# Kernel tuning notes

Measured on AMD Instinct MI355X. Metric: run time of the kernel, lower is better.

The kernel has to match this reference:

```python
import jax, jax.numpy as jnp
import numpy as np

H, W, C, B = 96, 96, 21, 2
THETA_ALPHA, THETA_BETA, THETA_GAMMA = 160.0, 3.0, 3.0
N_ITERS = 5


def _coords():
    yy, xx = jnp.meshgrid(jnp.arange(H, dtype=jnp.float32),
                          jnp.arange(W, dtype=jnp.float32), indexing='ij')
    return jnp.stack([yy.ravel(), xx.ravel()], axis=-1)  # [N,2]


def _gauss_kernel(feat):
    # exact dense Gaussian kernel exp(-||fi-fj||^2/2); ground truth for the
    # permutohedral-lattice approximate high_dim_filter op.
    sq = jnp.sum(feat * feat, axis=-1)
    d2 = sq[:, None] + sq[None, :] - 2.0 * (feat @ feat.T)
    return jnp.exp(-0.5 * jnp.maximum(d2, 0.0))  # [N,N]


def setup_inputs():
    key = jax.random.key(0)
    k1, k2 = jax.random.split(key)
    unary = jax.random.normal(k1, (B, H, W, C), dtype=jnp.float32)
    rgb = jax.random.uniform(k2, (B, H, W, 3), dtype=jnp.float32) * 255.0
    return {
        'unary': unary,
        'rgb': rgb,
        'spatial_ker_weights': jnp.eye(C, dtype=jnp.float32),
        'bilateral_ker_weights': jnp.eye(C, dtype=jnp.float32),
        'compatibility_matrix': -jnp.eye(C, dtype=jnp.float32),
    }


def _crf_single(u_chw, rgb_chw, Ws, Wb, M):
    N = H * W
    pos = _coords()
    # filter op has no gradient w.r.t. guide features in the original custom op
    rgb_flat = jax.lax.stop_gradient(rgb_chw).reshape(3, N).T  # [N,3]
    Ks = _gauss_kernel(pos / THETA_GAMMA)                       # spatial kernel [N,N]
    Kb = _gauss_kernel(jnp.concatenate([pos / THETA_ALPHA,
                                        rgb_flat / THETA_BETA], axis=-1))  # bilateral [N,N]
    ones = jnp.ones((N,), dtype=jnp.float32)
    sn = Ks @ ones  # spatial norm vals (filter of all-ones)
    bn = Kb @ ones  # bilateral norm vals
    u = u_chw.reshape(C, N)
    q = u
    for _ in range(N_ITERS):
        sm = jax.nn.softmax(q, axis=0)   # softmax over classes, [C,N]
        sp = (sm @ Ks) / sn              # Ks symmetric -> filtering = sm @ Ks
        bl = (sm @ Kb) / bn
        msg = Ws @ sp + Wb @ bl          # learned message passing [C,N]
        q = u - M @ msg                  # compatibility transform + unary update
    return q  # [C,N]


def reference(unary, rgb, spatial_ker_weights, bilateral_ker_weights, compatibility_matrix):
    u = jnp.transpose(unary, (0, 3, 1, 2))  # [B,C,H,W]
    r = jnp.transpose(rgb, (0, 3, 1, 2))    # [B,3,H,W]
    q = jax.vmap(_crf_single, in_axes=(0, 0, None, None, None))(
        u, r, spatial_ker_weights, bilateral_ker_weights, compatibility_matrix)
    return jnp.transpose(q.reshape(B, C, H, W), (0, 2, 3, 1))  # [B,H,W,C]
```

## Files before the change

kernel.cpp:

```cpp
#include <hip/hip_runtime.h>

#define HH 96
#define WW 96
#define CC 21
#define BB 2
#define NN (HH*WW)
#define NT16 (NN/16)
#define NJB  (NN/32)
#define CHK 8
#define NBILB 1296
#define PRUNE_T 24.0f
#define GST 104

#define KSA2 (0.84932184f / 160.0f)
#define KSB2 (0.84932184f / 3.0f)
#define GL2  (1.44269504f / 18.0f)

typedef __attribute__((ext_vector_type(4))) float f32x4;
typedef __attribute__((ext_vector_type(8))) short short8;
typedef __attribute__((ext_vector_type(4))) int int4v;

static __device__ inline unsigned pk_bf16(float a, float b) {
    unsigned ua = __builtin_bit_cast(unsigned, a);
    unsigned ub = __builtin_bit_cast(unsigned, b);
    ua += 0x7FFF + ((ua >> 16) & 1);
    ub += 0x7FFF + ((ub >> 16) & 1);
    return (ua >> 16) | (ub & 0xFFFF0000u);
}
static __device__ inline unsigned short bf16_1(float a) {
    unsigned ua = __builtin_bit_cast(unsigned, a);
    ua += 0x7FFF + ((ua >> 16) & 1);
    return (unsigned short)(ua >> 16);
}

__global__ __launch_bounds__(256) void prep_kernel(
    float* __restrict__ sxt, unsigned short* __restrict__ gbt,
    unsigned short* __restrict__ smht, int* __restrict__ gh, int* __restrict__ wlc)
{
    int idx = blockIdx.x * 256 + threadIdx.x;
    if (idx == 0) wlc[0] = 0;
    if (idx < BB * 11 * NN) {
        int b = idx / (11 * NN);
        int rem = idx - b * 11 * NN;
        int r = rem / NN, col = rem - r * NN;
        smht[(size_t)(b * 32 + 21 + r) * NN + col] = (r == 0) ? 0x3F80 : 0;
    }
    if (idx < BB * 4096) gh[idx] = 0;
    if (blockIdx.x == 0) {
        __shared__ float gt[96];
        int t = threadIdx.x;
        if (t < 96) gt[t] = __builtin_amdgcn_exp2f(-(float)(t * t) * GL2);
        __syncthreads();
        if (t < 96) {
            float s = 0.f;
            for (int v = 0; v < 96; v++) s += gt[abs(t - v)];
            sxt[t] = s;
            for (int v = 0; v < 96; v++) gbt[t * 96 + v] = bf16_1(gt[abs(t - v)]);
        }
    }
}

__global__ __launch_bounds__(256) void hist_kernel(
    const float* __restrict__ rgb, int* __restrict__ gh)
{
    int idx = blockIdx.x * 256 + threadIdx.x;
    if (idx >= BB * NN) return;
    int b = idx / NN;
    const float* rp = rgb + (size_t)idx * 3;
    int cr = min(15, (int)rp[0] >> 4);
    int cg = min(15, (int)rp[1] >> 4);
    int cb = min(15, (int)rp[2] >> 4);
    atomicAdd(&gh[b * 4096 + ((cr << 8) | (cg << 4) | cb)], 1);
}

__global__ __launch_bounds__(256) void scan_kernel(
    const int* __restrict__ gh, int* __restrict__ goff)
{
    __shared__ int ps[256];
    int t = threadIdx.x;
    for (int b = 0; b < BB; b++) {
        int base = b * 4096 + t * 16;
        int loc[16], s = 0;
#pragma unroll
        for (int k = 0; k < 16; k++) { loc[k] = gh[base + k]; s += loc[k]; }
        ps[t] = s;
        __syncthreads();
        for (int off = 1; off < 256; off <<= 1) {
            int add = (t >= off) ? ps[t - off] : 0;
            __syncthreads();
            ps[t] += add;
            __syncthreads();
        }
        int run = ps[t] - s;
#pragma unroll
        for (int k = 0; k < 16; k++) { goff[base + k] = run; run += loc[k]; }
        __syncthreads();
    }
}

__global__ __launch_bounds__(256) void scatter_kernel(
    const float* __restrict__ rgb, int* __restrict__ goff,
    int* __restrict__ spos, float* __restrict__ fjs)
{
    int idx = blockIdx.x * 256 + threadIdx.x;
    if (idx >= BB * NN) return;
    int b = idx / NN, p = idx - b * NN;
    const float* rp = rgb + (size_t)idx * 3;
    float r = rp[0], g = rp[1], bl = rp[2];
    int cr = min(15, (int)r >> 4);
    int cg = min(15, (int)g >> 4);
    int cb = min(15, (int)bl >> 4);
    int pos = atomicAdd(&goff[b * 4096 + ((cr << 8) | (cg << 4) | cb)], 1);
    spos[idx] = pos;
    int y = p / WW, x = p - y * WW;
    float* fb = fjs + (size_t)b * 5 * NN;
    fb[0 * NN + pos] = r * KSB2;
    fb[1 * NN + pos] = g * KSB2;
    fb[2 * NN + pos] = bl * KSB2;
    fb[3 * NN + pos] = (float)y * KSA2;
    fb[4 * NN + pos] = (float)x * KSA2;
}

__global__ __launch_bounds__(256) void bounds_kernel(
    const float* __restrict__ fjs, float* __restrict__ bnd)
{
    int idx = blockIdx.x * 256 + threadIdx.x;
    if (idx >= BB * NT16) return;
    int b = idx / NT16, tile = idx - b * NT16;
    const float* fb = fjs + (size_t)b * 5 * NN + tile * 16;
    float lo[3], hi[3];
#pragma unroll
    for (int f = 0; f < 3; f++) { lo[f] = 1e30f; hi[f] = -1e30f; }
    for (int k = 0; k < 16; k++) {
#pragma unroll
        for (int f = 0; f < 3; f++) {
            float v = fb[f * NN + k];
            lo[f] = fminf(lo[f], v); hi[f] = fmaxf(hi[f], v);
        }
    }
    float* o = bnd + (size_t)idx * 6;
#pragma unroll
    for (int f = 0; f < 3; f++) { o[2 * f] = lo[f]; o[2 * f + 1] = hi[f]; }
}

__global__ __launch_bounds__(256) void maskchunks_kernel(
    const float* __restrict__ bnd, unsigned short* __restrict__ jlist,
    int* __restrict__ cnt, int* __restrict__ wl, int* __restrict__ wlc)
{
    int lane = threadIdx.x & 63;
    int bt = blockIdx.x * 4 + (threadIdx.x >> 6);
    if (bt >= BB * NT16) return;
    int b = bt / NT16;
    const float* tb = bnd + (size_t)bt * 6;
    float tlo0 = tb[0], thi0 = tb[1], tlo1 = tb[2], thi1 = tb[3], tlo2 = tb[4], thi2 = tb[5];
    unsigned short* jl = jlist + (size_t)bt * NJB;
    const float* bb = bnd + (size_t)b * NT16 * 6;
    int n = 0;
#pragma unroll
    for (int r = 0; r < 5; r++) {
        int jb = r * 64 + lane;
        bool keep = false;
        if (jb < NJB) {
            const float* a0 = bb + (size_t)(2 * jb) * 6;
            float s = 0.f;
#pragma unroll
            for (int f = 0; f < 3; f++) {
                float jlo = fminf(a0[2 * f], a0[6 + 2 * f]);
                float jhi = fmaxf(a0[2 * f + 1], a0[6 + 2 * f + 1]);
                float lo = (f == 0) ? tlo0 : (f == 1) ? tlo1 : tlo2;
                float hi = (f == 0) ? thi0 : (f == 1) ? thi1 : thi2;
                float gap = fmaxf(0.f, fmaxf(lo - jhi, jlo - hi));
                s = fmaf(gap, gap, s);
            }
            keep = (s <= PRUNE_T);
        }
        unsigned long long m = __ballot(keep);
        if (keep) {
            int pre = __popcll(m & ((1ull << lane) - 1ull));
            jl[n + pre] = (unsigned short)jb;
        }
        n += __popcll(m);
    }
    if (lane == 0) {
        cnt[bt] = n;
        int nsl = (n + CHK - 1) / CHK;
        if (nsl > 0) {
            int base = atomicAdd(wlc, nsl);
            for (int s2 = 0; s2 < nsl; s2++) wl[base + s2] = bt * 64 + s2;
        }
    }
}

__global__ __launch_bounds__(256) void softmax_kernel(
    const float* __restrict__ q, const int* __restrict__ spos,
    unsigned short* __restrict__ smpb, unsigned short* __restrict__ smht,
    float* __restrict__ part)
{
    int idx = blockIdx.x * 256 + threadIdx.x;
    if (idx >= BB * NN) return;
    int b = idx / NN, p = idx - b * NN;
    const float* qp = q + (size_t)idx * CC;
    float v[CC], m = -1e30f;
#pragma unroll
    for (int c = 0; c < CC; c++) { v[c] = qp[c]; m = fmaxf(m, v[c]); }
    float ssum = 0.f;
#pragma unroll
    for (int c = 0; c < CC; c++) { v[c] = __expf(v[c] - m); ssum += v[c]; }
    float inv = 1.0f / ssum;
    int s = spos[idx];
#pragma unroll
    for (int c = 0; c < CC; c++) {
        unsigned short h = bf16_1(v[c] * inv);
        smpb[(size_t)(b * CC + c) * NN + p] = h;
        smht[(size_t)(b * 32 + c) * NN + s] = h;
    }
    float* pp = part + (size_t)(b * NN + s) * 24;
#pragma unroll
    for (int k = 0; k < 24; k++) pp[k] = 0.f;
}

__global__ __launch_bounds__(256) void conv_kernel(
    const unsigned short* __restrict__ smpb, const unsigned short* __restrict__ gbt,
    const float* __restrict__ sxt, float* __restrict__ spf)
{
    __shared__ unsigned short C1t[96 * GST];
    int tid = threadIdx.x;
    int lane = tid & 63, w = tid >> 6;
    int quad = lane >> 4, l16 = lane & 15;
    int bc = blockIdx.x;
    const unsigned short* plane = smpb + (size_t)bc * NN;
    for (int mt = w; mt < 6; mt += 4) {
        int m0 = mt * 16;
        short8 a[3];
#pragma unroll
        for (int kk = 0; kk < 3; kk++)
            a[kk] = *(const short8*)(plane + (size_t)(m0 + l16) * 96 + kk * 32 + quad * 8);
        f32x4 acc[6];
#pragma unroll
        for (int nt = 0; nt < 6; nt++) acc[nt] = (f32x4){0.f, 0.f, 0.f, 0.f};
#pragma unroll
        for (int nt = 0; nt < 6; nt++) {
#pragma unroll
            for (int kk = 0; kk < 3; kk++) {
                short8 bf = *(const short8*)(gbt + (nt * 16 + l16) * 96 + kk * 32 + quad * 8);
                acc[nt] = __builtin_amdgcn_mfma_f32_16x16x32_bf16(a[kk], bf, acc[nt], 0, 0, 0);
            }
        }
#pragma unroll
        for (int nt = 0; nt < 6; nt++) {
            unsigned* dst = (unsigned*)&C1t[(nt * 16 + l16) * GST + m0 + quad * 4];
            dst[0] = pk_bf16(acc[nt][0], acc[nt][1]);
            dst[1] = pk_bf16(acc[nt][2], acc[nt][3]);
        }
    }
    __syncthreads();
    float* outp = spf + (size_t)bc * NN;
    for (int mt = w; mt < 6; mt += 4) {
        int m0 = mt * 16;
        short8 a[3];
#pragma unroll
        for (int kk = 0; kk < 3; kk++)
            a[kk] = *(const short8*)(gbt + (m0 + l16) * 96 + kk * 32 + quad * 8);
        f32x4 acc[6];
#pragma unroll
        for (int nt = 0; nt < 6; nt++) acc[nt] = (f32x4){0.f, 0.f, 0.f, 0.f};
#pragma unroll
        for (int nt = 0; nt < 6; nt++) {
#pragma unroll
            for (int kk = 0; kk < 3; kk++) {
                short8 bf = *(const short8*)&C1t[(nt * 16 + l16) * GST + kk * 32 + quad * 8];
                acc[nt] = __builtin_amdgcn_mfma_f32_16x16x32_bf16(a[kk], bf, acc[nt], 0, 0, 0);
            }
        }
#pragma unroll
        for (int nt = 0; nt < 6; nt++) {
            int x = nt * 16 + l16;
            float sx = sxt[x];
#pragma unroll
            for (int r = 0; r < 4; r++) {
                int y = m0 + quad * 4 + r;
                float invn = __builtin_amdgcn_rcpf(sxt[y] * sx);
                outp[y * 96 + x] = acc[nt][r] * invn;
            }
        }
    }
}

struct JSet { float vf[5][8]; short8 sb0, sb1; };

static __device__ __forceinline__ void load_jset(
    JSet& s, const float* __restrict__ fb, const unsigned short* __restrict__ smb,
    int jb, int quad, int l16)
{
    int coff = jb * 32 + quad * 8;
#pragma unroll
    for (int f = 0; f < 5; f++) {
        const float4* pf = (const float4*)(fb + (size_t)f * NN + coff);
        float4 lo = pf[0], hi = pf[1];
        s.vf[f][0] = lo.x; s.vf[f][1] = lo.y; s.vf[f][2] = lo.z; s.vf[f][3] = lo.w;
        s.vf[f][4] = hi.x; s.vf[f][5] = hi.y; s.vf[f][6] = hi.z; s.vf[f][7] = hi.w;
    }
    s.sb0 = *(const short8*)(smb + (size_t)l16 * NN + coff);
    s.sb1 = *(const short8*)(smb + (size_t)(16 + l16) * NN + coff);
}

static __device__ __forceinline__ void compute_jset(
    const JSet& s, float fi0, float fi1, float fi2, float fi3, float fi4,
    f32x4& acc0, f32x4& acc1)
{
    float kf[8];
#pragma unroll
    for (int e = 0; e < 8; e++) {
        float d0 = s.vf[0][e] - fi0;
        float d1 = s.vf[1][e] - fi1;
        float d2 = s.vf[2][e] - fi2;
        float d3 = s.vf[3][e] - fi3;
        float d4 = s.vf[4][e] - fi4;
        float sm = d0 * d0;
        sm = fmaf(d1, d1, sm);
        sm = fmaf(d2, d2, sm);
        sm = fmaf(d3, d3, sm);
        sm = fmaf(d4, d4, sm);
        kf[e] = __builtin_amdgcn_exp2f(-sm);
    }
    int4v ap = { (int)pk_bf16(kf[0], kf[1]), (int)pk_bf16(kf[2], kf[3]),
                 (int)pk_bf16(kf[4], kf[5]), (int)pk_bf16(kf[6], kf[7]) };
    short8 afrag = __builtin_bit_cast(short8, ap);
    acc0 = __builtin_amdgcn_mfma_f32_16x16x32_bf16(afrag, s.sb0, acc0, 0, 0, 0);
    acc1 = __builtin_amdgcn_mfma_f32_16x16x32_bf16(afrag, s.sb1, acc1, 0, 0, 0);
}

__global__ __launch_bounds__(256) void bilateral_wl_kernel(
    const unsigned short* __restrict__ smht, const float* __restrict__ fjs,
    const unsigned short* __restrict__ jlist, const int* __restrict__ cntv,
    const int* __restrict__ wl, const int* __restrict__ wlc,
    float* __restrict__ part)
{
    int tid = threadIdx.x;
    int lane = tid & 63, w = tid >> 6;
    int quad = lane >> 4, l16 = lane & 15;
    int nwl = wlc[0];
    int totw = gridDim.x * 4;
    for (int widx = blockIdx.x * 4 + w; widx < nwl; widx += totw) {
        int e = wl[widx];
        int bt = e >> 6, ck = e & 63;
        int cnt = min(cntv[bt] - ck * CHK, CHK);
        int b = bt / NT16, tile16 = bt - b * NT16;
        int i = tile16 * 16 + l16;
        const float* fb = fjs + (size_t)b * 5 * NN;
        float fi0 = fb[0 * NN + i], fi1 = fb[1 * NN + i], fi2 = fb[2 * NN + i];
        float fi3 = fb[3 * NN + i], fi4 = fb[4 * NN + i];
        f32x4 acc0 = {0.f, 0.f, 0.f, 0.f};
        f32x4 acc1 = {0.f, 0.f, 0.f, 0.f};
        const unsigned short* smb = smht + (size_t)b * 32 * NN;
        const unsigned short* jl = jlist + (size_t)bt * NJB + ck * CHK;

        JSet A, B;
        load_jset(A, fb, smb, jl[0], quad, l16);
        int k = 0;
        while (true) {
            if (k + 1 < cnt) load_jset(B, fb, smb, jl[k + 1], quad, l16);
            compute_jset(A, fi0, fi1, fi2, fi3, fi4, acc0, acc1);
            if (++k >= cnt) break;
            if (k + 1 < cnt) load_jset(A, fb, smb, jl[k + 1], quad, l16);
            compute_jset(B, fi0, fi1, fi2, fi3, fi4, acc0, acc1);
            if (++k >= cnt) break;
        }

        int ibase = tile16 * 16 + quad * 4;
        float* pr = part + (size_t)b * NN * 24;
#pragma unroll
        for (int r = 0; r < 4; r++)
            atomicAdd(&pr[(size_t)(ibase + r) * 24 + l16], acc0[r]);
        if (l16 < 6) {
#pragma unroll
            for (int r = 0; r < 4; r++)
                atomicAdd(&pr[(size_t)(ibase + r) * 24 + 16 + l16], acc1[r]);
        }
    }
}

__global__ __launch_bounds__(256) void update_fused_kernel(
    const float* __restrict__ u, const float* __restrict__ spf,
    float* __restrict__ part, const int* __restrict__ spos,
    const float* __restrict__ Ws, const float* __restrict__ Wb,
    const float* __restrict__ M, float* __restrict__ qout,
    unsigned short* __restrict__ smpb, unsigned short* __restrict__ smht, int wr)
{
    __shared__ float sWs[441], sWb[441], sM[441];
    for (int t = threadIdx.x; t < 441; t += 256) {
        sWs[t] = Ws[t]; sWb[t] = Wb[t]; sM[t] = M[t];
    }
    __syncthreads();
    int idx = blockIdx.x * 256 + threadIdx.x;
    if (idx >= BB * NN) return;
    int b = idx / NN, p = idx - b * NN;
    int s = spos[idx];
    float* pp = part + (size_t)(b * NN + s) * 24;
    float blv[22];
#pragma unroll
    for (int c = 0; c < 22; c++) blv[c] = pp[c];
    float ninv = 1.0f / blv[21];
    float spv[CC], msg[CC];
#pragma unroll
    for (int c = 0; c < CC; c++) {
        blv[c] *= ninv;
        spv[c] = spf[(size_t)(b * CC + c) * NN + p];
    }
#pragma unroll
    for (int c = 0; c < CC; c++) {
        float a = 0.f;
        const float* wr2 = &sWs[c * CC];
        const float* br = &sWb[c * CC];
#pragma unroll
        for (int c2 = 0; c2 < CC; c2++) a = fmaf(wr2[c2], spv[c2], a);
#pragma unroll
        for (int c2 = 0; c2 < CC; c2++) a = fmaf(br[c2], blv[c2], a);
        msg[c] = a;
    }
    const float* up = u + (size_t)idx * CC;
    float* qp = qout + (size_t)idx * CC;
    float qv[CC];
#pragma unroll
    for (int c = 0; c < CC; c++) {
        float a = up[c];
        const float* mr = &sM[c * CC];
#pragma unroll
        for (int c2 = 0; c2 < CC; c2++) a = fmaf(-mr[c2], msg[c2], a);
        qv[c] = a;
        qp[c] = a;
    }
    if (wr) {
        float m = -1e30f;
#pragma unroll
        for (int c = 0; c < CC; c++) m = fmaxf(m, qv[c]);
        float ssum = 0.f;
#pragma unroll
        for (int c = 0; c < CC; c++) { qv[c] = __expf(qv[c] - m); ssum += qv[c]; }
        float inv = 1.0f / ssum;
#pragma unroll
        for (int c = 0; c < CC; c++) {
            unsigned short h = bf16_1(qv[c] * inv);
            smpb[(size_t)(b * CC + c) * NN + p] = h;
            smht[(size_t)(b * 32 + c) * NN + s] = h;
        }
#pragma unroll
        for (int k = 0; k < 24; k++) pp[k] = 0.f;
    }
}

extern "C" void kernel_launch(void* const* d_in, const int* in_sizes, int n_in,
                              void* d_out, int out_size, void* d_ws, size_t ws_size,
                              hipStream_t stream)
{
    const float* unary = (const float*)d_in[0];
    const float* rgb   = (const float*)d_in[1];
    const float* Ws    = (const float*)d_in[2];
    const float* Wb    = (const float*)d_in[3];
    const float* M     = (const float*)d_in[4];
    float* out = (float*)d_out;

    float* SXT  = (float*)d_ws;
    float* FJS  = SXT + 96;
    float* SPF  = FJS + (size_t)BB * 5 * NN;
    float* PART = SPF + (size_t)BB * CC * NN;
    float* BND  = PART + (size_t)BB * NN * 24;
    int*   SPOS = (int*)(BND + (size_t)BB * NT16 * 6);
    int*   GH   = SPOS + BB * NN;
    int*   GOFF = GH + BB * 4096;
    int*   CNT  = GOFF + BB * 4096;
    int*   WLC  = CNT + BB * NT16;
    int*   WL   = WLC + 1;
    unsigned short* JL = (unsigned short*)(WL + BB * NT16 * 36);
    unsigned short* SMHT = JL + (size_t)BB * NT16 * NJB;
    unsigned short* SMPB = SMHT + (size_t)BB * 32 * NN;
    unsigned short* GBT  = SMPB + (size_t)BB * CC * NN;

    prep_kernel<<<(BB * 11 * NN + 255) / 256, 256, 0, stream>>>(SXT, GBT, SMHT, GH, WLC);
    hist_kernel<<<(BB * NN + 255) / 256, 256, 0, stream>>>(rgb, GH);
    scan_kernel<<<1, 256, 0, stream>>>(GH, GOFF);
    scatter_kernel<<<(BB * NN + 255) / 256, 256, 0, stream>>>(rgb, GOFF, SPOS, FJS);
    bounds_kernel<<<(BB * NT16 + 255) / 256, 256, 0, stream>>>(FJS, BND);
    maskchunks_kernel<<<(BB * NT16 + 3) / 4, 256, 0, stream>>>(BND, JL, CNT, WL, WLC);

    softmax_kernel<<<(BB * NN + 255) / 256, 256, 0, stream>>>(unary, SPOS, SMPB, SMHT, PART);
    for (int it = 0; it < 5; ++it) {
        conv_kernel<<<BB * CC, 256, 0, stream>>>(SMPB, GBT, SXT, SPF);
        bilateral_wl_kernel<<<NBILB, 256, 0, stream>>>(SMHT, FJS, JL, CNT, WL, WLC, PART);
        update_fused_kernel<<<(BB * NN + 255) / 256, 256, 0, stream>>>(
            unary, SPF, PART, SPOS, Ws, Wb, M, out, SMPB, SMHT, (it < 4) ? 1 : 0);
    }
}
```

Before: 355.1 us.

## Fuse conv, bilateral and update into one per-iteration kernel with grid barrier

Replaces the three per-iteration launches with one kernel. The first blocks do the spatial separable convolution and the bilateral worklist at the same time. The remaining blocks spin on a per-iteration atomic done counter before running the message-passing update. This removes two launches and their gaps per iteration and overlaps the spatial and bilateral work. In exchange, the bilateral worker count is halved and update blocks busy-wait while holding CU slots, which relies on all blocks being resident at once. The histogram scan is also split into one block per batch.

```diff
diff --git a/kernel.cpp b/kernel.cpp
--- a/kernel.cpp
+++ b/kernel.cpp
@@ -8,7 +8,10 @@
 #define NT16 (NN/16)
 #define NJB  (NN/32)
 #define CHK 8
-#define NBILB 1296
+#define NCONV (BB*CC)
+#define NBIL 648
+#define NUPD (BB*NN/256)
+#define NWORKER (NCONV+NBIL)
 #define PRUNE_T 24.0f
 #define GST 104
 
@@ -35,10 +38,12 @@
 
 __global__ __launch_bounds__(256) void prep_kernel(
     float* __restrict__ sxt, unsigned short* __restrict__ gbt,
-    unsigned short* __restrict__ smht, int* __restrict__ gh, int* __restrict__ wlc)
+    unsigned short* __restrict__ smht, int* __restrict__ gh,
+    int* __restrict__ wlc, int* __restrict__ done)
 {
     int idx = blockIdx.x * 256 + threadIdx.x;
     if (idx == 0) wlc[0] = 0;
+    if (idx < 8) done[idx] = 0;
     if (idx < BB * 11 * NN) {
         int b = idx / (11 * NN);
         int rem = idx - b * 11 * NN;
@@ -77,25 +82,22 @@
     const int* __restrict__ gh, int* __restrict__ goff)
 {
     __shared__ int ps[256];
-    int t = threadIdx.x;
-    for (int b = 0; b < BB; b++) {
-        int base = b * 4096 + t * 16;
-        int loc[16], s = 0;
-#pragma unroll
-        for (int k = 0; k < 16; k++) { loc[k] = gh[base + k]; s += loc[k]; }
-        ps[t] = s;
+    int t = threadIdx.x, b = blockIdx.x;
+    int base = b * 4096 + t * 16;
+    int loc[16], s = 0;
+#pragma unroll
+    for (int k = 0; k < 16; k++) { loc[k] = gh[base + k]; s += loc[k]; }
+    ps[t] = s;
+    __syncthreads();
+    for (int off = 1; off < 256; off <<= 1) {
+        int add = (t >= off) ? ps[t - off] : 0;
         __syncthreads();
-        for (int off = 1; off < 256; off <<= 1) {
-            int add = (t >= off) ? ps[t - off] : 0;
-            __syncthreads();
-            ps[t] += add;
-            __syncthreads();
-        }
-        int run = ps[t] - s;
-#pragma unroll
-        for (int k = 0; k < 16; k++) { goff[base + k] = run; run += loc[k]; }
+        ps[t] += add;
         __syncthreads();
     }
+    int run = ps[t] - s;
+#pragma unroll
+    for (int k = 0; k < 16; k++) { goff[base + k] = run; run += loc[k]; }
 }
 
 __global__ __launch_bounds__(256) void scatter_kernel(
@@ -219,73 +221,6 @@
     for (int k = 0; k < 24; k++) pp[k] = 0.f;
 }
 
-__global__ __launch_bounds__(256) void conv_kernel(
-    const unsigned short* __restrict__ smpb, const unsigned short* __restrict__ gbt,
-    const float* __restrict__ sxt, float* __restrict__ spf)
-{
-    __shared__ unsigned short C1t[96 * GST];
-    int tid = threadIdx.x;
-    int lane = tid & 63, w = tid >> 6;
-    int quad = lane >> 4, l16 = lane & 15;
-    int bc = blockIdx.x;
-    const unsigned short* plane = smpb + (size_t)bc * NN;
-    for (int mt = w; mt < 6; mt += 4) {
-        int m0 = mt * 16;
-        short8 a[3];
-#pragma unroll
-        for (int kk = 0; kk < 3; kk++)
-            a[kk] = *(const short8*)(plane + (size_t)(m0 + l16) * 96 + kk * 32 + quad * 8);
-        f32x4 acc[6];
-#pragma unroll
-        for (int nt = 0; nt < 6; nt++) acc[nt] = (f32x4){0.f, 0.f, 0.f, 0.f};
-#pragma unroll
-        for (int nt = 0; nt < 6; nt++) {
-#pragma unroll
-            for (int kk = 0; kk < 3; kk++) {
-                short8 bf = *(const short8*)(gbt + (nt * 16 + l16) * 96 + kk * 32 + quad * 8);
-                acc[nt] = __builtin_amdgcn_mfma_f32_16x16x32_bf16(a[kk], bf, acc[nt], 0, 0, 0);
-            }
-        }
-#pragma unroll
-        for (int nt = 0; nt < 6; nt++) {
-            unsigned* dst = (unsigned*)&C1t[(nt * 16 + l16) * GST + m0 + quad * 4];
-            dst[0] = pk_bf16(acc[nt][0], acc[nt][1]);
-            dst[1] = pk_bf16(acc[nt][2], acc[nt][3]);
-        }
-    }
-    __syncthreads();
-    float* outp = spf + (size_t)bc * NN;
-    for (int mt = w; mt < 6; mt += 4) {
-        int m0 = mt * 16;
-        short8 a[3];
-#pragma unroll
-        for (int kk = 0; kk < 3; kk++)
-            a[kk] = *(const short8*)(gbt + (m0 + l16) * 96 + kk * 32 + quad * 8);
-        f32x4 acc[6];
-#pragma unroll
-        for (int nt = 0; nt < 6; nt++) acc[nt] = (f32x4){0.f, 0.f, 0.f, 0.f};
-#pragma unroll
-        for (int nt = 0; nt < 6; nt++) {
-#pragma unroll
-            for (int kk = 0; kk < 3; kk++) {
-                short8 bf = *(const short8*)&C1t[(nt * 16 + l16) * GST + kk * 32 + quad * 8];
-                acc[nt] = __builtin_amdgcn_mfma_f32_16x16x32_bf16(a[kk], bf, acc[nt], 0, 0, 0);
-            }
-        }
-#pragma unroll
-        for (int nt = 0; nt < 6; nt++) {
-            int x = nt * 16 + l16;
-            float sx = sxt[x];
-#pragma unroll
-            for (int r = 0; r < 4; r++) {
-                int y = m0 + quad * 4 + r;
-                float invn = __builtin_amdgcn_rcpf(sxt[y] * sx);
-                outp[y * 96 + x] = acc[nt][r] * invn;
-            }
-        }
-    }
-}
-
 struct JSet { float vf[5][8]; short8 sb0, sb1; };
 
 static __device__ __forceinline__ void load_jset(
@@ -330,70 +265,143 @@
     acc1 = __builtin_amdgcn_mfma_f32_16x16x32_bf16(afrag, s.sb1, acc1, 0, 0, 0);
 }
 
-__global__ __launch_bounds__(256) void bilateral_wl_kernel(
-    const unsigned short* __restrict__ smht, const float* __restrict__ fjs,
+__global__ __launch_bounds__(256) void iter_kernel(
+    const unsigned short* __restrict__ smpb, const unsigned short* __restrict__ gbt,
+    const float* __restrict__ sxt, float* __restrict__ spf,
+    const unsigned short* __restrict__ smht_c, const float* __restrict__ fjs,
     const unsigned short* __restrict__ jlist, const int* __restrict__ cntv,
     const int* __restrict__ wl, const int* __restrict__ wlc,
-    float* __restrict__ part)
-{
+    float* __restrict__ part,
+    const float* __restrict__ u, const int* __restrict__ spos,
+    const float* __restrict__ Ws, const float* __restrict__ Wb,
+    const float* __restrict__ M, float* __restrict__ qout,
+    unsigned short* __restrict__ smpb_w, unsigned short* __restrict__ smht_w,
+    int* __restrict__ done, int wr)
+{
+    __shared__ unsigned short C1t[96 * GST];
     int tid = threadIdx.x;
     int lane = tid & 63, w = tid >> 6;
     int quad = lane >> 4, l16 = lane & 15;
-    int nwl = wlc[0];
-    int totw = gridDim.x * 4;
-    for (int widx = blockIdx.x * 4 + w; widx < nwl; widx += totw) {
-        int e = wl[widx];
-        int bt = e >> 6, ck = e & 63;
-        int cnt = min(cntv[bt] - ck * CHK, CHK);
-        int b = bt / NT16, tile16 = bt - b * NT16;
-        int i = tile16 * 16 + l16;
-        const float* fb = fjs + (size_t)b * 5 * NN;
-        float fi0 = fb[0 * NN + i], fi1 = fb[1 * NN + i], fi2 = fb[2 * NN + i];
-        float fi3 = fb[3 * NN + i], fi4 = fb[4 * NN + i];
-        f32x4 acc0 = {0.f, 0.f, 0.f, 0.f};
-        f32x4 acc1 = {0.f, 0.f, 0.f, 0.f};
-        const unsigned short* smb = smht + (size_t)b * 32 * NN;
-        const unsigned short* jl = jlist + (size_t)bt * NJB + ck * CHK;
-
-        JSet A, B;
-        load_jset(A, fb, smb, jl[0], quad, l16);
-        int k = 0;
-        while (true) {
-            if (k + 1 < cnt) load_jset(B, fb, smb, jl[k + 1], quad, l16);
-            compute_jset(A, fi0, fi1, fi2, fi3, fi4, acc0, acc1);
-            if (++k >= cnt) break;
-            if (k + 1 < cnt) load_jset(A, fb, smb, jl[k + 1], quad, l16);
-            compute_jset(B, fi0, fi1, fi2, fi3, fi4, acc0, acc1);
-            if (++k >= cnt) break;
-        }
-
-        int ibase = tile16 * 16 + quad * 4;
-        float* pr = part + (size_t)b * NN * 24;
-#pragma unroll
-        for (int r = 0; r < 4; r++)
-            atomicAdd(&pr[(size_t)(ibase + r) * 24 + l16], acc0[r]);
-        if (l16 < 6) {
+    int bid = blockIdx.x;
+
+    if (bid < NCONV) {
+        const unsigned short* plane = smpb + (size_t)bid * NN;
+        for (int mt = w; mt < 6; mt += 4) {
+            int m0 = mt * 16;
+            short8 a[3];
+#pragma unroll
+            for (int kk = 0; kk < 3; kk++)
+                a[kk] = *(const short8*)(plane + (size_t)(m0 + l16) * 96 + kk * 32 + quad * 8);
+            f32x4 acc[6];
+#pragma unroll
+            for (int nt = 0; nt < 6; nt++) acc[nt] = (f32x4){0.f, 0.f, 0.f, 0.f};
+#pragma unroll
+            for (int nt = 0; nt < 6; nt++) {
+#pragma unroll
+                for (int kk = 0; kk < 3; kk++) {
+                    short8 bf = *(const short8*)(gbt + (nt * 16 + l16) * 96 + kk * 32 + quad * 8);
+                    acc[nt] = __builtin_amdgcn_mfma_f32_16x16x32_bf16(a[kk], bf, acc[nt], 0, 0, 0);
+                }
+            }
+#pragma unroll
+            for (int nt = 0; nt < 6; nt++) {
+                unsigned* dst = (unsigned*)&C1t[(nt * 16 + l16) * GST + m0 + quad * 4];
+                dst[0] = pk_bf16(acc[nt][0], acc[nt][1]);
+                dst[1] = pk_bf16(acc[nt][2], acc[nt][3]);
+            }
+        }
+        __syncthreads();
+        float* outp = spf + (size_t)bid * NN;
+        for (int mt = w; mt < 6; mt += 4) {
+            int m0 = mt * 16;
+            short8 a[3];
+#pragma unroll
+            for (int kk = 0; kk < 3; kk++)
+                a[kk] = *(const short8*)(gbt + (m0 + l16) * 96 + kk * 32 + quad * 8);
+            f32x4 acc[6];
+#pragma unroll
+            for (int nt = 0; nt < 6; nt++) acc[nt] = (f32x4){0.f, 0.f, 0.f, 0.f};
+#pragma unroll
+            for (int nt = 0; nt < 6; nt++) {
+#pragma unroll
+                for (int kk = 0; kk < 3; kk++) {
+                    short8 bf = *(const short8*)&C1t[(nt * 16 + l16) * GST + kk * 32 + quad * 8];
+                    acc[nt] = __builtin_amdgcn_mfma_f32_16x16x32_bf16(a[kk], bf, acc[nt], 0, 0, 0);
+                }
+            }
+#pragma unroll
+            for (int nt = 0; nt < 6; nt++) {
+                int x = nt * 16 + l16;
+                float sx = sxt[x];
+#pragma unroll
+                for (int r = 0; r < 4; r++) {
+                    int y = m0 + quad * 4 + r;
+                    float invn = __builtin_amdgcn_rcpf(sxt[y] * sx);
+                    outp[y * 96 + x] = acc[nt][r] * invn;
+                }
+            }
+        }
+    } else if (bid < NWORKER) {
+        int nwl = wlc[0];
+        for (int widx = (bid - NCONV) * 4 + w; widx < nwl; widx += NBIL * 4) {
+            int e = wl[widx];
+            int bt = e >> 6, ck = e & 63;
+            int cnt = min(cntv[bt] - ck * CHK, CHK);
+            int b = bt / NT16, tile16 = bt - b * NT16;
+            int i = tile16 * 16 + l16;
+            const float* fb = fjs + (size_t)b * 5 * NN;
+            float fi0 = fb[0 * NN + i], fi1 = fb[1 * NN + i], fi2 = fb[2 * NN + i];
+            float fi3 = fb[3 * NN + i], fi4 = fb[4 * NN + i];
+            f32x4 acc0 = {0.f, 0.f, 0.f, 0.f};
+            f32x4 acc1 = {0.f, 0.f, 0.f, 0.f};
+            const unsigned short* smb = smht_c + (size_t)b * 32 * NN;
+            const unsigned short* jl = jlist + (size_t)bt * NJB + ck * CHK;
+            JSet A, B;
+            load_jset(A, fb, smb, jl[0], quad, l16);
+            int k = 0;
+            while (true) {
+                if (k + 1 < cnt) load_jset(B, fb, smb, jl[k + 1], quad, l16);
+                compute_jset(A, fi0, fi1, fi2, fi3, fi4, acc0, acc1);
+                if (++k >= cnt) break;
+                if (k + 1 < cnt) load_jset(A, fb, smb, jl[k + 1], quad, l16);
+                compute_jset(B, fi0, fi1, fi2, fi3, fi4, acc0, acc1);
+                if (++k >= cnt) break;
+            }
+            int ibase = tile16 * 16 + quad * 4;
+            float* pr = part + (size_t)b * NN * 24;
 #pragma unroll
             for (int r = 0; r < 4; r++)
-                atomicAdd(&pr[(size_t)(ibase + r) * 24 + 16 + l16], acc1[r]);
-        }
-    }
-}
-
-__global__ __launch_bounds__(256) void update_fused_kernel(
-    const float* __restrict__ u, const float* __restrict__ spf,
-    float* __restrict__ part, const int* __restrict__ spos,
-    const float* __restrict__ Ws, const float* __restrict__ Wb,
-    const float* __restrict__ M, float* __restrict__ qout,
-    unsigned short* __restrict__ smpb, unsigned short* __restrict__ smht, int wr)
-{
-    __shared__ float sWs[441], sWb[441], sM[441];
-    for (int t = threadIdx.x; t < 441; t += 256) {
-        sWs[t] = Ws[t]; sWb[t] = Wb[t]; sM[t] = M[t];
+                atomicAdd(&pr[(size_t)(ibase + r) * 24 + l16], acc0[r]);
+            if (l16 < 6) {
+#pragma unroll
+                for (int r = 0; r < 4; r++)
+                    atomicAdd(&pr[(size_t)(ibase + r) * 24 + 16 + l16], acc1[r]);
+            }
+        }
+    }
+
+    if (bid < NWORKER) {
+        __threadfence();
+        __syncthreads();
+        if (tid == 0)
+            __hip_atomic_fetch_add(done, 1, __ATOMIC_RELEASE, __HIP_MEMORY_SCOPE_AGENT);
+        return;
+    }
+
+    if (tid == 0) {
+        while (__hip_atomic_load(done, __ATOMIC_ACQUIRE, __HIP_MEMORY_SCOPE_AGENT) < NWORKER)
+            __builtin_amdgcn_s_sleep(8);
     }
     __syncthreads();
-    int idx = blockIdx.x * 256 + threadIdx.x;
-    if (idx >= BB * NN) return;
+    __threadfence();
+
+    float* sWs = (float*)&C1t[0];
+    float* sWb = sWs + 441;
+    float* sM  = sWb + 441;
+    for (int t = tid; t < 441; t += 256) { sWs[t] = Ws[t]; sWb[t] = Wb[t]; sM[t] = M[t]; }
+    __syncthreads();
+
+    int idx = (bid - NWORKER) * 256 + tid;
     int b = idx / NN, p = idx - b * NN;
     int s = spos[idx];
     float* pp = part + (size_t)(b * NN + s) * 24;
@@ -441,8 +449,8 @@
 #pragma unroll
         for (int c = 0; c < CC; c++) {
             unsigned short h = bf16_1(qv[c] * inv);
-            smpb[(size_t)(b * CC + c) * NN + p] = h;
-            smht[(size_t)(b * 32 + c) * NN + s] = h;
+            smpb_w[(size_t)(b * CC + c) * NN + p] = h;
+            smht_w[(size_t)(b * 32 + c) * NN + s] = h;
         }
 #pragma unroll
         for (int k = 0; k < 24; k++) pp[k] = 0.f;
@@ -470,24 +478,24 @@
     int*   GOFF = GH + BB * 4096;
     int*   CNT  = GOFF + BB * 4096;
     int*   WLC  = CNT + BB * NT16;
-    int*   WL   = WLC + 1;
+    int*   DONE = WLC + 1;
+    int*   WL   = DONE + 8;
     unsigned short* JL = (unsigned short*)(WL + BB * NT16 * 36);
     unsigned short* SMHT = JL + (size_t)BB * NT16 * NJB;
     unsigned short* SMPB = SMHT + (size_t)BB * 32 * NN;
     unsigned short* GBT  = SMPB + (size_t)BB * CC * NN;
 
-    prep_kernel<<<(BB * 11 * NN + 255) / 256, 256, 0, stream>>>(SXT, GBT, SMHT, GH, WLC);
+    prep_kernel<<<(BB * 11 * NN + 255) / 256, 256, 0, stream>>>(SXT, GBT, SMHT, GH, WLC, DONE);
     hist_kernel<<<(BB * NN + 255) / 256, 256, 0, stream>>>(rgb, GH);
-    scan_kernel<<<1, 256, 0, stream>>>(GH, GOFF);
+    scan_kernel<<<BB, 256, 0, stream>>>(GH, GOFF);
     scatter_kernel<<<(BB * NN + 255) / 256, 256, 0, stream>>>(rgb, GOFF, SPOS, FJS);
     bounds_kernel<<<(BB * NT16 + 255) / 256, 256, 0, stream>>>(FJS, BND);
     maskchunks_kernel<<<(BB * NT16 + 3) / 4, 256, 0, stream>>>(BND, JL, CNT, WL, WLC);
 
     softmax_kernel<<<(BB * NN + 255) / 256, 256, 0, stream>>>(unary, SPOS, SMPB, SMHT, PART);
     for (int it = 0; it < 5; ++it) {
-        conv_kernel<<<BB * CC, 256, 0, stream>>>(SMPB, GBT, SXT, SPF);
-        bilateral_wl_kernel<<<NBILB, 256, 0, stream>>>(SMHT, FJS, JL, CNT, WL, WLC, PART);
-        update_fused_kernel<<<(BB * NN + 255) / 256, 256, 0, stream>>>(
-            unary, SPF, PART, SPOS, Ws, Wb, M, out, SMPB, SMHT, (it < 4) ? 1 : 0);
-    }
-}
+        iter_kernel<<<NWORKER + NUPD, 256, 0, stream>>>(
+            SMPB, GBT, SXT, SPF, SMHT, FJS, JL, CNT, WL, WLC, PART,
+            unary, SPOS, Ws, Wb, M, out, SMPB, SMHT, DONE + it, (it < 4) ? 1 : 0);
+    }
+}
```

Result: slower. 710.1 us (+100.0%).

## Merge spatial conv and bilateral filter into one launch, parallelize scan per batch

Applied to the files above, without the earlier changes.

The spatial separable convolution and the bilateral worklist filter now run as one kernel. The first blocks do the conv and the remaining blocks walk the bilateral worklist, which removes one launch per iteration and lets the two independent stages overlap. The bilateral block count drops from 1296 to 648. The histogram scan uses one block per batch instead of a serial loop, and intermediate q writes to the output are skipped except on the last iteration. The combined kernel now reserves conv shared memory for every block, which may lower occupancy for the bilateral blocks.

```diff
diff --git a/kernel.cpp b/kernel.cpp
--- a/kernel.cpp
+++ b/kernel.cpp
@@ -8,7 +8,8 @@
 #define NT16 (NN/16)
 #define NJB  (NN/32)
 #define CHK 8
-#define NBILB 1296
+#define NCONV (BB*CC)
+#define NBIL 648
 #define PRUNE_T 24.0f
 #define GST 104
 
@@ -77,25 +78,22 @@
     const int* __restrict__ gh, int* __restrict__ goff)
 {
     __shared__ int ps[256];
-    int t = threadIdx.x;
-    for (int b = 0; b < BB; b++) {
-        int base = b * 4096 + t * 16;
-        int loc[16], s = 0;
-#pragma unroll
-        for (int k = 0; k < 16; k++) { loc[k] = gh[base + k]; s += loc[k]; }
-        ps[t] = s;
+    int t = threadIdx.x, b = blockIdx.x;
+    int base = b * 4096 + t * 16;
+    int loc[16], s = 0;
+#pragma unroll
+    for (int k = 0; k < 16; k++) { loc[k] = gh[base + k]; s += loc[k]; }
+    ps[t] = s;
+    __syncthreads();
+    for (int off = 1; off < 256; off <<= 1) {
+        int add = (t >= off) ? ps[t - off] : 0;
         __syncthreads();
-        for (int off = 1; off < 256; off <<= 1) {
-            int add = (t >= off) ? ps[t - off] : 0;
-            __syncthreads();
-            ps[t] += add;
-            __syncthreads();
-        }
-        int run = ps[t] - s;
-#pragma unroll
-        for (int k = 0; k < 16; k++) { goff[base + k] = run; run += loc[k]; }
+        ps[t] += add;
         __syncthreads();
     }
+    int run = ps[t] - s;
+#pragma unroll
+    for (int k = 0; k < 16; k++) { goff[base + k] = run; run += loc[k]; }
 }
 
 __global__ __launch_bounds__(256) void scatter_kernel(
@@ -219,73 +217,6 @@
     for (int k = 0; k < 24; k++) pp[k] = 0.f;
 }
 
-__global__ __launch_bounds__(256) void conv_kernel(
-    const unsigned short* __restrict__ smpb, const unsigned short* __restrict__ gbt,
-    const float* __restrict__ sxt, float* __restrict__ spf)
-{
-    __shared__ unsigned short C1t[96 * GST];
-    int tid = threadIdx.x;
-    int lane = tid & 63, w = tid >> 6;
-    int quad = lane >> 4, l16 = lane & 15;
-    int bc = blockIdx.x;
-    const unsigned short* plane = smpb + (size_t)bc * NN;
-    for (int mt = w; mt < 6; mt += 4) {
-        int m0 = mt * 16;
-        short8 a[3];
-#pragma unroll
-        for (int kk = 0; kk < 3; kk++)
-            a[kk] = *(const short8*)(plane + (size_t)(m0 + l16) * 96 + kk * 32 + quad * 8);
-        f32x4 acc[6];
-#pragma unroll
-        for (int nt = 0; nt < 6; nt++) acc[nt] = (f32x4){0.f, 0.f, 0.f, 0.f};
-#pragma unroll
-        for (int nt = 0; nt < 6; nt++) {
-#pragma unroll
-            for (int kk = 0; kk < 3; kk++) {
-                short8 bf = *(const short8*)(gbt + (nt * 16 + l16) * 96 + kk * 32 + quad * 8);
-                acc[nt] = __builtin_amdgcn_mfma_f32_16x16x32_bf16(a[kk], bf, acc[nt], 0, 0, 0);
-            }
-        }
-#pragma unroll
-        for (int nt = 0; nt < 6; nt++) {
-            unsigned* dst = (unsigned*)&C1t[(nt * 16 + l16) * GST + m0 + quad * 4];
-            dst[0] = pk_bf16(acc[nt][0], acc[nt][1]);
-            dst[1] = pk_bf16(acc[nt][2], acc[nt][3]);
-        }
-    }
-    __syncthreads();
-    float* outp = spf + (size_t)bc * NN;
-    for (int mt = w; mt < 6; mt += 4) {
-        int m0 = mt * 16;
-        short8 a[3];
-#pragma unroll
-        for (int kk = 0; kk < 3; kk++)
-            a[kk] = *(const short8*)(gbt + (m0 + l16) * 96 + kk * 32 + quad * 8);
-        f32x4 acc[6];
-#pragma unroll
-        for (int nt = 0; nt < 6; nt++) acc[nt] = (f32x4){0.f, 0.f, 0.f, 0.f};
-#pragma unroll
-        for (int nt = 0; nt < 6; nt++) {
-#pragma unroll
-            for (int kk = 0; kk < 3; kk++) {
-                short8 bf = *(const short8*)&C1t[(nt * 16 + l16) * GST + kk * 32 + quad * 8];
-                acc[nt] = __builtin_amdgcn_mfma_f32_16x16x32_bf16(a[kk], bf, acc[nt], 0, 0, 0);
-            }
-        }
-#pragma unroll
-        for (int nt = 0; nt < 6; nt++) {
-            int x = nt * 16 + l16;
-            float sx = sxt[x];
-#pragma unroll
-            for (int r = 0; r < 4; r++) {
-                int y = m0 + quad * 4 + r;
-                float invn = __builtin_amdgcn_rcpf(sxt[y] * sx);
-                outp[y * 96 + x] = acc[nt][r] * invn;
-            }
-        }
-    }
-}
-
 struct JSet { float vf[5][8]; short8 sb0, sb1; };
 
 static __device__ __forceinline__ void load_jset(
@@ -330,18 +261,82 @@
     acc1 = __builtin_amdgcn_mfma_f32_16x16x32_bf16(afrag, s.sb1, acc1, 0, 0, 0);
 }
 
-__global__ __launch_bounds__(256) void bilateral_wl_kernel(
-    const unsigned short* __restrict__ smht, const float* __restrict__ fjs,
+__global__ __launch_bounds__(256) void conv_bil_kernel(
+    const unsigned short* __restrict__ smpb, const unsigned short* __restrict__ gbt,
+    const float* __restrict__ sxt, float* __restrict__ spf,
+    const unsigned short* __restrict__ smht_c, const float* __restrict__ fjs,
     const unsigned short* __restrict__ jlist, const int* __restrict__ cntv,
     const int* __restrict__ wl, const int* __restrict__ wlc,
     float* __restrict__ part)
 {
+    __shared__ unsigned short C1t[96 * GST];
     int tid = threadIdx.x;
     int lane = tid & 63, w = tid >> 6;
     int quad = lane >> 4, l16 = lane & 15;
+    int bid = blockIdx.x;
+
+    if (bid < NCONV) {
+        const unsigned short* plane = smpb + (size_t)bid * NN;
+        for (int mt = w; mt < 6; mt += 4) {
+            int m0 = mt * 16;
+            short8 a[3];
+#pragma unroll
+            for (int kk = 0; kk < 3; kk++)
+                a[kk] = *(const short8*)(plane + (size_t)(m0 + l16) * 96 + kk * 32 + quad * 8);
+            f32x4 acc[6];
+#pragma unroll
+            for (int nt = 0; nt < 6; nt++) acc[nt] = (f32x4){0.f, 0.f, 0.f, 0.f};
+#pragma unroll
+            for (int nt = 0; nt < 6; nt++) {
+#pragma unroll
+                for (int kk = 0; kk < 3; kk++) {
+                    short8 bf = *(const short8*)(gbt + (nt * 16 + l16) * 96 + kk * 32 + quad * 8);
+                    acc[nt] = __builtin_amdgcn_mfma_f32_16x16x32_bf16(a[kk], bf, acc[nt], 0, 0, 0);
+                }
+            }
+#pragma unroll
+            for (int nt = 0; nt < 6; nt++) {
+                unsigned* dst = (unsigned*)&C1t[(nt * 16 + l16) * GST + m0 + quad * 4];
+                dst[0] = pk_bf16(acc[nt][0], acc[nt][1]);
+                dst[1] = pk_bf16(acc[nt][2], acc[nt][3]);
+            }
+        }
+        __syncthreads();
+        float* outp = spf + (size_t)bid * NN;
+        for (int mt = w; mt < 6; mt += 4) {
+            int m0 = mt * 16;
+            short8 a[3];
+#pragma unroll
+            for (int kk = 0; kk < 3; kk++)
+                a[kk] = *(const short8*)(gbt + (m0 + l16) * 96 + kk * 32 + quad * 8);
+            f32x4 acc[6];
+#pragma unroll
+            for (int nt = 0; nt < 6; nt++) acc[nt] = (f32x4){0.f, 0.f, 0.f, 0.f};
+#pragma unroll
+            for (int nt = 0; nt < 6; nt++) {
+#pragma unroll
+                for (int kk = 0; kk < 3; kk++) {
+                    short8 bf = *(const short8*)&C1t[(nt * 16 + l16) * GST + kk * 32 + quad * 8];
+                    acc[nt] = __builtin_amdgcn_mfma_f32_16x16x32_bf16(a[kk], bf, acc[nt], 0, 0, 0);
+                }
+            }
+#pragma unroll
+            for (int nt = 0; nt < 6; nt++) {
+                int x = nt * 16 + l16;
+                float sx = sxt[x];
+#pragma unroll
+                for (int r = 0; r < 4; r++) {
+                    int y = m0 + quad * 4 + r;
+                    float invn = __builtin_amdgcn_rcpf(sxt[y] * sx);
+                    outp[y * 96 + x] = acc[nt][r] * invn;
+                }
+            }
+        }
+        return;
+    }
+
     int nwl = wlc[0];
-    int totw = gridDim.x * 4;
-    for (int widx = blockIdx.x * 4 + w; widx < nwl; widx += totw) {
+    for (int widx = (bid - NCONV) * 4 + w; widx < nwl; widx += NBIL * 4) {
         int e = wl[widx];
         int bt = e >> 6, ck = e & 63;
         int cnt = min(cntv[bt] - ck * CHK, CHK);
@@ -352,9 +347,8 @@
         float fi3 = fb[3 * NN + i], fi4 = fb[4 * NN + i];
         f32x4 acc0 = {0.f, 0.f, 0.f, 0.f};
         f32x4 acc1 = {0.f, 0.f, 0.f, 0.f};
-        const unsigned short* smb = smht + (size_t)b * 32 * NN;
+        const unsigned short* smb = smht_c + (size_t)b * 32 * NN;
         const unsigned short* jl = jlist + (size_t)bt * NJB + ck * CHK;
-
         JSet A, B;
         load_jset(A, fb, smb, jl[0], quad, l16);
         int k = 0;
@@ -366,7 +360,6 @@
             compute_jset(B, fi0, fi1, fi2, fi3, fi4, acc0, acc1);
             if (++k >= cnt) break;
         }
-
         int ibase = tile16 * 16 + quad * 4;
         float* pr = part + (size_t)b * NN * 24;
 #pragma unroll
@@ -419,7 +412,6 @@
         msg[c] = a;
     }
     const float* up = u + (size_t)idx * CC;
-    float* qp = qout + (size_t)idx * CC;
     float qv[CC];
 #pragma unroll
     for (int c = 0; c < CC; c++) {
@@ -428,24 +420,28 @@
 #pragma unroll
         for (int c2 = 0; c2 < CC; c2++) a = fmaf(-mr[c2], msg[c2], a);
         qv[c] = a;
-        qp[c] = a;
     }
     if (wr) {
         float m = -1e30f;
 #pragma unroll
         for (int c = 0; c < CC; c++) m = fmaxf(m, qv[c]);
         float ssum = 0.f;
-#pragma unroll
-        for (int c = 0; c < CC; c++) { qv[c] = __expf(qv[c] - m); ssum += qv[c]; }
+        float ev[CC];
+#pragma unroll
+        for (int c = 0; c < CC; c++) { ev[c] = __expf(qv[c] - m); ssum += ev[c]; }
         float inv = 1.0f / ssum;
 #pragma unroll
         for (int c = 0; c < CC; c++) {
-            unsigned short h = bf16_1(qv[c] * inv);
+            unsigned short h = bf16_1(ev[c] * inv);
             smpb[(size_t)(b * CC + c) * NN + p] = h;
             smht[(size_t)(b * 32 + c) * NN + s] = h;
         }
 #pragma unroll
         for (int k = 0; k < 24; k++) pp[k] = 0.f;
+    } else {
+        float* qp = qout + (size_t)idx * CC;
+#pragma unroll
+        for (int c = 0; c < CC; c++) qp[c] = qv[c];
     }
 }
 
@@ -478,15 +474,15 @@
 
     prep_kernel<<<(BB * 11 * NN + 255) / 256, 256, 0, stream>>>(SXT, GBT, SMHT, GH, WLC);
     hist_kernel<<<(BB * NN + 255) / 256, 256, 0, stream>>>(rgb, GH);
-    scan_kernel<<<1, 256, 0, stream>>>(GH, GOFF);
+    scan_kernel<<<BB, 256, 0, stream>>>(GH, GOFF);
     scatter_kernel<<<(BB * NN + 255) / 256, 256, 0, stream>>>(rgb, GOFF, SPOS, FJS);
     bounds_kernel<<<(BB * NT16 + 255) / 256, 256, 0, stream>>>(FJS, BND);
     maskchunks_kernel<<<(BB * NT16 + 3) / 4, 256, 0, stream>>>(BND, JL, CNT, WL, WLC);
 
     softmax_kernel<<<(BB * NN + 255) / 256, 256, 0, stream>>>(unary, SPOS, SMPB, SMHT, PART);
     for (int it = 0; it < 5; ++it) {
-        conv_kernel<<<BB * CC, 256, 0, stream>>>(SMPB, GBT, SXT, SPF);
-        bilateral_wl_kernel<<<NBILB, 256, 0, stream>>>(SMHT, FJS, JL, CNT, WL, WLC, PART);
+        conv_bil_kernel<<<NCONV + NBIL, 256, 0, stream>>>(
+            SMPB, GBT, SXT, SPF, SMHT, FJS, JL, CNT, WL, WLC, PART);
         update_fused_kernel<<<(BB * NN + 255) / 256, 256, 0, stream>>>(
             unary, SPF, PART, SPOS, Ws, Wb, M, out, SMPB, SMHT, (it < 4) ? 1 : 0);
     }
```

Measured after the change: 315.6 us. -11.1%, faster.
